# Optimization experiments

Hardware: AMD Instinct MI355X
Metric: run time of the kernel (lower is better)

Reference implementation:

```python
import jax, jax.numpy as jnp
import numpy as np

N_STEPS = 5
N_ETYPES = 4
N_GRAPHS = 64
HEADS = 2
N, E, D = 50000, 600000, 128
C = 32


def setup_inputs() -> dict:
    key = jax.random.key(0)
    ks = jax.random.split(key, 24)
    s = 0.08  # param scale to keep activations well-conditioned
    return {
        "in_feat1": jax.random.normal(ks[0], (N, D), jnp.float32),
        "in_feat2": jax.random.normal(ks[1], (N, D), jnp.float32),
        "src1": jax.random.randint(ks[2], (E,), 0, N, jnp.int32),
        "dst1": jax.random.randint(ks[3], (E,), 0, N, jnp.int32),
        "etype1": jax.random.randint(ks[4], (E,), 0, N_ETYPES, jnp.int32),
        "gid1": jnp.sort(jax.random.randint(ks[5], (N,), 0, N_GRAPHS, jnp.int32)),
        "src2": jax.random.randint(ks[6], (E,), 0, N, jnp.int32),
        "dst2": jax.random.randint(ks[7], (E,), 0, N, jnp.int32),
        "etype2": jax.random.randint(ks[8], (E,), 0, N_ETYPES, jnp.int32),
        "gid2": jnp.sort(jax.random.randint(ks[9], (N,), 0, N_GRAPHS, jnp.int32)),
        "W_et": jax.random.normal(ks[10], (N_ETYPES, D, D), jnp.float32) * s,
        "b_et": jax.random.normal(ks[11], (N_ETYPES, D), jnp.float32) * s,
        "W_ih": jax.random.normal(ks[12], (3 * D, D), jnp.float32) * s,
        "W_hh": jax.random.normal(ks[13], (3 * D, D), jnp.float32) * s,
        "b_ih": jax.random.normal(ks[14], (3 * D,), jnp.float32) * s,
        "b_hh": jax.random.normal(ks[15], (3 * D,), jnp.float32) * s,
        "W_fc": jax.random.normal(ks[16], (HEADS * D, D), jnp.float32) * s,
        "attn_l": jax.random.normal(ks[17], (HEADS, D), jnp.float32) * s,
        "attn_r": jax.random.normal(ks[18], (HEADS, D), jnp.float32) * s,
        "gat_bias": jax.random.normal(ks[19], (HEADS * D,), jnp.float32) * s,
        "W_cls": jax.random.normal(ks[20], (C, D), jnp.float32) * s,
        "b_cls": jax.random.normal(ks[21], (C,), jnp.float32) * s,
    }


def _ggann(feat, src, dst, etype, gid,
           W_et, b_et, W_ih, W_hh, b_ih, b_hh,
           W_fc, attn_l, attn_r, gat_bias, W_cls, b_cls):
    n = feat.shape[0]
    h = feat  # in_feats == out_feats -> no zero-padding needed
    # ---- GatedGraphConv: n_steps of per-etype message passing + GRU ----
    for _ in range(N_STEPS):
        # per-etype linear on all nodes: [K, N, D]
        t = jnp.einsum('kod,nd->kno', W_et, h) + b_et[:, None, :]
        msg = t[etype, src]                         # [E, D] gather by (etype, src)
        a = jax.ops.segment_sum(msg, dst, num_segments=n)  # [N, D]
        # GRUCell(a, h)
        gi = a @ W_ih.T + b_ih                      # [N, 3D]
        gh = h @ W_hh.T + b_hh
        i_r, i_z, i_n = jnp.split(gi, 3, axis=1)
        h_r, h_z, h_n = jnp.split(gh, 3, axis=1)
        r = jax.nn.sigmoid(i_r + h_r)
        z = jax.nn.sigmoid(i_z + h_z)
        nn_ = jnp.tanh(i_n + r * h_n)
        h = (1.0 - z) * nn_ + z * h
    # F.normalize (L2 over dim=1) then sigmoid
    h = h / jnp.maximum(jnp.linalg.norm(h, axis=1, keepdims=True), 1e-12)
    h = jax.nn.sigmoid(h)
    # ---- GATConv (num_heads=2) ----
    zft = (h @ W_fc.T).reshape(n, HEADS, D)         # [N, H, D]
    el = jnp.sum(zft * attn_l[None], axis=-1)       # [N, H]
    er = jnp.sum(zft * attn_r[None], axis=-1)
    e = jax.nn.leaky_relu(el[src] + er[dst], 0.2)   # [E, H]
    m = jax.ops.segment_max(e, dst, num_segments=n)
    ex = jnp.exp(e - m[dst])
    den = jax.ops.segment_sum(ex, dst, num_segments=n)
    alpha = ex / den[dst]                           # edge softmax per dst, per head
    rst = jax.ops.segment_sum(alpha[:, :, None] * zft[src], dst, num_segments=n)
    rst = rst + gat_bias.reshape(1, HEADS, D)
    h = jax.nn.relu(rst)                            # [N, H, D] (dropout = eval identity)
    # ---- mean_nodes per graph + classify ----
    sums = jax.ops.segment_sum(h, gid, num_segments=N_GRAPHS)      # [B, H, D]
    cnt = jax.ops.segment_sum(jnp.ones((n, 1, 1), h.dtype), gid, num_segments=N_GRAPHS)
    hg = sums / jnp.maximum(cnt, 1.0)
    return hg @ W_cls.T + b_cls                     # [B, H, C]


def reference(in_feat1, in_feat2, src1, dst1, etype1, gid1,
              src2, dst2, etype2, gid2,
              W_et, b_et, W_ih, W_hh, b_ih, b_hh,
              W_fc, attn_l, attn_r, gat_bias, W_cls, b_cls):
    params = (W_et, b_et, W_ih, W_hh, b_ih, b_hh,
              W_fc, attn_l, attn_r, gat_bias, W_cls, b_cls)
    h1 = _ggann(in_feat1, src1, dst1, etype1, gid1, *params)  # [B, H, C]
    h2 = _ggann(in_feat2, src2, dst2, etype2, gid2, *params)
    # F.pairwise_distance(p=2, eps=1e-6) over last dim -> [B, H]
    dist = jnp.linalg.norm(h1 - h2 + 1e-6, axis=-1)
    return jax.nn.softmax(dist, axis=1)             # softmax over the 2 heads
```

## Files before the change

kernel.cpp:

```cpp
#include <hip/hip_runtime.h>
#include <math.h>

#define D 128
#define NG 64
#define NG2 128
#define NSTEPS 5

using short8 = __attribute__((ext_vector_type(8))) short;
using f32x4  = __attribute__((ext_vector_type(4))) float;
using f32x2  = __attribute__((ext_vector_type(2))) float;

__device__ __forceinline__ float sigf(float x) {
  float e = __expf(-fabsf(x));
  float inv = __fdividef(1.f, 1.f + e);
  return x >= 0.f ? inv : e * inv;
}
__device__ __forceinline__ float tanhf_fast(float x) {
  float e = __expf(-2.f * fabsf(x));
  float r = (1.f - e) * __fdividef(1.f, 1.f + e);
  return x >= 0.f ? r : -r;
}
__device__ __forceinline__ float lrelu(float x) { return x > 0.f ? x : 0.2f * x; }
__device__ __forceinline__ short f2bf(float x) {
  unsigned u = __float_as_uint(x);
  u += 0x7fff + ((u >> 16) & 1);
  return (short)(u >> 16);
}
__device__ __forceinline__ unsigned pk2(float x, float y) {
  return ((unsigned)(unsigned short)f2bf(y) << 16) | (unsigned short)f2bf(x);
}
__device__ __forceinline__ float bflo(unsigned v) { return __uint_as_float(v << 16); }
__device__ __forceinline__ float bfhi(unsigned v) { return __uint_as_float(v & 0xffff0000u); }
__device__ __forceinline__ float bf2f(short s) {
  return __uint_as_float(((unsigned)(unsigned short)s) << 16);
}
__device__ __forceinline__ unsigned char f2fp8(float x) {
  int p = __builtin_amdgcn_cvt_pk_fp8_f32(x, x, 0, false);
  return (unsigned char)(p & 0xff);
}

__device__ __forceinline__ void packK128(const float* __restrict__ W,
                                         short* __restrict__ P, int i) {
  int j = i & 7;
  int lane = (i >> 3) & 63;
  int kt = (i >> 9) & 3;
  int nt = i >> 11;
  int c = nt * 16 + (lane & 15);
  int k = kt * 32 + ((lane >> 4) << 3) + j;
  P[i] = f2bf(W[c * 128 + k]);
}
__device__ __forceinline__ void packA512f(const float* __restrict__ W_et,
                                          short* __restrict__ P, int i) {
  int j = i & 7;
  int lane = (i >> 3) & 63;
  int kt = (i >> 9) & 15;
  int nt = i >> 13;
  int c = nt * 16 + (lane & 15);
  int k = kt * 32 + ((lane >> 4) << 3) + j;
  P[i] = f2bf(W_et[(k >> 7) * 16384 + c * 128 + (k & 127)]);
}

__global__ __launch_bounds__(256) void k_setup(const float* __restrict__ W_et,
    const float* __restrict__ W_ih, const float* __restrict__ W_hh,
    const float* __restrict__ W_fc, const float* __restrict__ f1,
    const float* __restrict__ f2, short* __restrict__ WaP, short* __restrict__ WihP,
    short* __restrict__ WhhP, short* __restrict__ WfcP, short* __restrict__ hb,
    unsigned char* __restrict__ hq,
    int* __restrict__ deg, int* __restrict__ gcnt, int N2, int Nd4) {
  const int sA = 65536, sB = 49152, sC = 49152, sD = 32768;
  int sE = N2, sF = NG2;
  long sG = 2L * Nd4;
  long tot = (long)(sA + sB + sC + sD) + sE + sF + sG;
  for (long ii = (long)blockIdx.x * blockDim.x + threadIdx.x; ii < tot;
       ii += (long)gridDim.x * blockDim.x) {
    long r = ii;
    if (r < sA) { packA512f(W_et, WaP, (int)r); continue; }
    r -= sA;
    if (r < sB) { packK128(W_ih, WihP, (int)r); continue; }
    r -= sB;
    if (r < sC) { packK128(W_hh, WhhP, (int)r); continue; }
    r -= sC;
    if (r < sD) { packK128(W_fc, WfcP, (int)r); continue; }
    r -= sD;
    if (r < sE) { deg[r] = 0; continue; }
    r -= sE;
    if (r < sF) { gcnt[r] = 0; continue; }
    r -= sF;
    {
      int i = (int)r;
      float4 v = (i < Nd4) ? ((const float4*)f1)[i] : ((const float4*)f2)[i - Nd4];
      ((uint2*)hb)[i] = make_uint2(pk2(v.x, v.y), pk2(v.z, v.w));
      int q = __builtin_amdgcn_cvt_pk_fp8_f32(v.x, v.y, 0, false);
      q = __builtin_amdgcn_cvt_pk_fp8_f32(v.z, v.w, q, true);
      ((unsigned*)hq)[i] = (unsigned)q;
    }
  }
}

__global__ __launch_bounds__(256) void k_histgid(const int* __restrict__ dst1,
    const int* __restrict__ dst2, const int* __restrict__ gid1,
    const int* __restrict__ gid2, int E, int N, int* __restrict__ deg,
    int* __restrict__ gidc, int* __restrict__ gcnt, int EB, int N2) {
  __shared__ int cnt[NG2];
  if ((int)blockIdx.x < EB) {
    int slice = blockIdx.x & 7;
    int bls = blockIdx.x >> 3;
    int nbs = EB >> 3;
    int W = (N2 + 7) >> 3;
    int lo = slice * W, hi = lo + W;
    for (int e = bls * 256 + threadIdx.x; e < 2 * E; e += nbs * 256) {
      int d = (e < E) ? dst1[e] : dst2[e - E] + N;
      if (d >= lo && d < hi) atomicAdd(&deg[d], 1);
    }
  } else {
    int t = threadIdx.x;
    if (t < NG2) cnt[t] = 0;
    __syncthreads();
    int i = (blockIdx.x - EB) * 256 + t;
    if (i < 2 * N) {
      int g = (i < N) ? gid1[i] : gid2[i - N] + NG;
      gidc[i] = g;
      atomicAdd(&cnt[g], 1);
    }
    __syncthreads();
    if (t < NG2 && cnt[t]) atomicAdd(&gcnt[t], cnt[t]);
  }
}

__global__ __launch_bounds__(256) void k_scan_a(const int* __restrict__ deg, int n,
                                                int* __restrict__ bsum) {
  int base = blockIdx.x * 1024 + threadIdx.x * 4;
  int s = 0;
  if (base + 3 < n) {
    int4 v = *(const int4*)(deg + base);
    s = v.x + v.y + v.z + v.w;
  } else {
    for (int k = 0; k < 4; ++k) if (base + k < n) s += deg[base + k];
  }
  #pragma unroll
  for (int off = 32; off; off >>= 1) s += __shfl_xor(s, off);
  __shared__ int ws[4];
  if ((threadIdx.x & 63) == 0) ws[threadIdx.x >> 6] = s;
  __syncthreads();
  if (threadIdx.x == 0) bsum[blockIdx.x] = ws[0] + ws[1] + ws[2] + ws[3];
}

__global__ __launch_bounds__(1024) void k_scan_b(const int* __restrict__ bsum,
                                                 int* __restrict__ boffs, int nb) {
  int tid = threadIdx.x;
  int v = (tid < nb) ? bsum[tid] : 0;
  int lane = tid & 63, wv = tid >> 6;
  int x = v;
  #pragma unroll
  for (int off = 1; off < 64; off <<= 1) {
    int y = __shfl_up(x, off);
    if (lane >= off) x += y;
  }
  __shared__ int wsum[16];
  if (lane == 63) wsum[wv] = x;
  __syncthreads();
  if (tid < 16) {
    int u = wsum[tid];
    #pragma unroll
    for (int off = 1; off < 16; off <<= 1) {
      int y = __shfl_up(u, off);
      if (tid >= off) u += y;
    }
    wsum[tid] = u;
  }
  __syncthreads();
  int woff = wv ? wsum[wv - 1] : 0;
  if (tid < nb) boffs[tid] = woff + x - v;
}

__global__ __launch_bounds__(256) void k_scan_c(const int* __restrict__ deg,
    const int* __restrict__ boffs, int* __restrict__ row_ofs,
    int* __restrict__ cursor, int n) {
  int base = blockIdx.x * 1024 + threadIdx.x * 4;
  int v[4] = {0, 0, 0, 0};
  if (base + 3 < n) {
    int4 t = *(const int4*)(deg + base);
    v[0] = t.x; v[1] = t.y; v[2] = t.z; v[3] = t.w;
  } else {
    for (int k = 0; k < 4; ++k) if (base + k < n) v[k] = deg[base + k];
  }
  int s = v[0] + v[1] + v[2] + v[3];
  int lane = threadIdx.x & 63, wv = threadIdx.x >> 6;
  int x = s;
  #pragma unroll
  for (int off = 1; off < 64; off <<= 1) {
    int y = __shfl_up(x, off);
    if (lane >= off) x += y;
  }
  __shared__ int wsum[4];
  if (lane == 63) wsum[wv] = x;
  __syncthreads();
  int woff = 0;
  for (int w = 0; w < wv; ++w) woff += wsum[w];
  int run = boffs[blockIdx.x] + woff + x - s;
  #pragma unroll
  for (int k = 0; k < 4; ++k) {
    int i = base + k;
    if (i < n) {
      cursor[i] = run;
      run += v[k];
      row_ofs[i + 1] = run;
    }
  }
  if (blockIdx.x == 0 && threadIdx.x == 0) row_ofs[0] = 0;
}

__global__ __launch_bounds__(256) void k_scatter(const int* __restrict__ src1,
    const int* __restrict__ dst1, const int* __restrict__ ety1,
    const int* __restrict__ src2, const int* __restrict__ dst2,
    const int* __restrict__ ety2, int E, int N, int* __restrict__ cursor,
    int* __restrict__ csr_se, int N2) {
  int slice = blockIdx.x & 7;
  int bls = blockIdx.x >> 3;
  int nbs = gridDim.x >> 3;
  int W = (N2 + 7) >> 3;
  int lo = slice * W, hi = lo + W;
  for (int e = bls * 256 + threadIdx.x; e < 2 * E; e += nbs * 256) {
    int d = (e < E) ? dst1[e] : dst2[e - E] + N;
    if (d < lo || d >= hi) continue;
    int s, et;
    if (e < E) { s = src1[e]; et = ety1[e]; }
    else { s = src2[e - E] + N; et = ety2[e - E]; }
    int p = atomicAdd(&cursor[d], 1);
    csr_se[p] = (s << 10) + et;
  }
}

__global__ __launch_bounds__(1024) void k_aggemm(const unsigned char* __restrict__ hq,
    const int* __restrict__ row_ofs, const int* __restrict__ csr_se,
    const short* __restrict__ WaP, const float* __restrict__ b_et,
    short* __restrict__ ab, int M) {
  __shared__ short Stile[16 * 512];
  __shared__ float lcnt[16][4];
  int tid = threadIdx.x;
  int lane = tid & 63, wave = tid >> 6;
  int row0 = blockIdx.x * 16;

  int li = wave;
  int node = row0 + li;
  f32x2 A0 = {0.f, 0.f}, A1 = {0.f, 0.f}, A2 = {0.f, 0.f}, A3 = {0.f, 0.f};
  int c0 = 0, c1 = 0, c2 = 0, c3 = 0;
  const char* hqb = (const char*)hq;
  if (node < M) {
    int beg = row_ofs[node], end = row_ofs[node + 1];
    #define ACC(ET, V) do { \
        f32x2 t_ = __builtin_amdgcn_cvt_pk_f32_fp8((unsigned)(V), false); \
        if (ET == 0)      { A0 += t_; ++c0; } \
        else if (ET == 1) { A1 += t_; ++c1; } \
        else if (ET == 2) { A2 += t_; ++c2; } \
        else              { A3 += t_; ++c3; } } while (0)
    for (int base = beg; base < end; base += 64) {
      int nv = end - base; if (nv > 64) nv = 64;
      int r = (lane < nv) ? csr_se[base + lane] : 0;
      int j = 0;
      for (; j + 16 <= nv; j += 16) {
        int rr[16];
        #pragma unroll
        for (int k = 0; k < 16; ++k) rr[k] = __builtin_amdgcn_readlane(r, j + k);
        unsigned short v[16];
        #pragma unroll
        for (int k = 0; k < 16; ++k)
          v[k] = ((const unsigned short*)(hqb + (rr[k] >> 3)))[lane];
        #pragma unroll
        for (int k = 0; k < 16; ++k) ACC(rr[k] & 3, v[k]);
      }
      for (; j + 8 <= nv; j += 8) {
        int rr[8];
        #pragma unroll
        for (int k = 0; k < 8; ++k) rr[k] = __builtin_amdgcn_readlane(r, j + k);
        unsigned short v[8];
        #pragma unroll
        for (int k = 0; k < 8; ++k)
          v[k] = ((const unsigned short*)(hqb + (rr[k] >> 3)))[lane];
        #pragma unroll
        for (int k = 0; k < 8; ++k) ACC(rr[k] & 3, v[k]);
      }
      for (; j + 4 <= nv; j += 4) {
        int rr[4];
        #pragma unroll
        for (int k = 0; k < 4; ++k) rr[k] = __builtin_amdgcn_readlane(r, j + k);
        unsigned short v[4];
        #pragma unroll
        for (int k = 0; k < 4; ++k)
          v[k] = ((const unsigned short*)(hqb + (rr[k] >> 3)))[lane];
        #pragma unroll
        for (int k = 0; k < 4; ++k) ACC(rr[k] & 3, v[k]);
      }
      for (; j < nv; ++j) {
        int rr = __builtin_amdgcn_readlane(r, j);
        unsigned short v = ((const unsigned short*)(hqb + (rr >> 3)))[lane];
        ACC(rr & 3, v);
      }
    }
    #undef ACC
  }
  {
    int swz = (li & 7) << 4;
    unsigned* ld = (unsigned*)Stile;
    ld[(li * 1024 + ((lane * 4      ) ^ swz)) >> 2] = pk2(A0[0], A0[1]);
    ld[(li * 1024 + ((lane * 4 + 256) ^ swz)) >> 2] = pk2(A1[0], A1[1]);
    ld[(li * 1024 + ((lane * 4 + 512) ^ swz)) >> 2] = pk2(A2[0], A2[1]);
    ld[(li * 1024 + ((lane * 4 + 768) ^ swz)) >> 2] = pk2(A3[0], A3[1]);
    if (lane == 0) {
      lcnt[li][0] = (float)c0; lcnt[li][1] = (float)c1;
      lcnt[li][2] = (float)c2; lcnt[li][3] = (float)c3;
    }
  }
  __syncthreads();

  if (wave < 8) {
    int quad = lane >> 4, l15 = lane & 15;
    int swz = (l15 & 7) << 4;
    int nt = wave;
    f32x4 acc = {0.f, 0.f, 0.f, 0.f};
    #pragma unroll
    for (int kt = 0; kt < 16; ++kt) {
      int boff = l15 * 1024 + ((kt * 64 + quad * 16) ^ swz);
      short8 a = *(const short8*)((const char*)Stile + boff);
      short8 b = *(const short8*)(WaP + (((size_t)(nt * 16 + kt) * 64) + lane) * 8);
      acc = __builtin_amdgcn_mfma_f32_16x16x32_bf16(a, b, acc, 0, 0, 0);
    }
    int c = nt * 16 + l15;
    float be0 = b_et[c], be1 = b_et[128 + c], be2 = b_et[256 + c], be3 = b_et[384 + c];
    #pragma unroll
    for (int reg = 0; reg < 4; ++reg) {
      int lr = quad * 4 + reg;
      int r = row0 + lr;
      if (r < M) {
        float v = acc[reg] + lcnt[lr][0] * be0 + lcnt[lr][1] * be1
                           + lcnt[lr][2] * be2 + lcnt[lr][3] * be3;
        ab[(size_t)r * 128 + c] = f2bf(v);
      }
    }
  }
}

__global__ __launch_bounds__(256) void k_gru_mfma(const short* __restrict__ ab,
    short* __restrict__ hb, unsigned char* __restrict__ hq,
    const short* __restrict__ Pih, const short* __restrict__ Phh,
    const float* __restrict__ b_ih, const float* __restrict__ b_hh, int M) {
  int tid = threadIdx.x;
  int lane = tid & 63, wave = tid >> 6;
  int row0 = blockIdx.x * 128 + wave * 32;
  int quad = lane >> 4, l15 = lane & 15;
  short8 fa[2][4], fh[2][4];
  #pragma unroll
  for (int rt = 0; rt < 2; ++rt) {
    int ar = row0 + rt * 16 + l15; if (ar >= M) ar = M - 1;
    #pragma unroll
    for (int kt = 0; kt < 4; ++kt) {
      fa[rt][kt] = *(const short8*)(ab + (size_t)ar * 128 + kt * 32 + quad * 8);
      fh[rt][kt] = *(const short8*)(hb + (size_t)ar * 128 + kt * 32 + quad * 8);
    }
  }
  for (int nt = 0; nt < 8; ++nt) {
    f32x4 accr[2], accz[2], acci[2], acch[2];
    #pragma unroll
    for (int rt = 0; rt < 2; ++rt) {
      accr[rt] = {0.f,0.f,0.f,0.f}; accz[rt] = {0.f,0.f,0.f,0.f};
      acci[rt] = {0.f,0.f,0.f,0.f}; acch[rt] = {0.f,0.f,0.f,0.f};
    }
    #pragma unroll
    for (int kt = 0; kt < 4; ++kt) {
      size_t li = ((size_t)lane) * 8;
      short8 wr = *(const short8*)(Pih + ((size_t)((nt     ) * 4 + kt) * 64) * 8 + li);
      short8 wz = *(const short8*)(Pih + ((size_t)((nt +  8) * 4 + kt) * 64) * 8 + li);
      short8 wn = *(const short8*)(Pih + ((size_t)((nt + 16) * 4 + kt) * 64) * 8 + li);
      short8 ur = *(const short8*)(Phh + ((size_t)((nt     ) * 4 + kt) * 64) * 8 + li);
      short8 uz = *(const short8*)(Phh + ((size_t)((nt +  8) * 4 + kt) * 64) * 8 + li);
      short8 un = *(const short8*)(Phh + ((size_t)((nt + 16) * 4 + kt) * 64) * 8 + li);
      #pragma unroll
      for (int rt = 0; rt < 2; ++rt) {
        accr[rt] = __builtin_amdgcn_mfma_f32_16x16x32_bf16(fa[rt][kt], wr, accr[rt], 0, 0, 0);
        accr[rt] = __builtin_amdgcn_mfma_f32_16x16x32_bf16(fh[rt][kt], ur, accr[rt], 0, 0, 0);
        accz[rt] = __builtin_amdgcn_mfma_f32_16x16x32_bf16(fa[rt][kt], wz, accz[rt], 0, 0, 0);
        accz[rt] = __builtin_amdgcn_mfma_f32_16x16x32_bf16(fh[rt][kt], uz, accz[rt], 0, 0, 0);
        acci[rt] = __builtin_amdgcn_mfma_f32_16x16x32_bf16(fa[rt][kt], wn, acci[rt], 0, 0, 0);
        acch[rt] = __builtin_amdgcn_mfma_f32_16x16x32_bf16(fh[rt][kt], un, acch[rt], 0, 0, 0);
      }
    }
    int c = nt * 16 + l15;
    float bir = b_ih[c],      bhr = b_hh[c];
    float biz = b_ih[c+128],  bhz = b_hh[c+128];
    float bin_= b_ih[c+256],  bhn = b_hh[c+256];
    #pragma unroll
    for (int rt = 0; rt < 2; ++rt) {
      #pragma unroll
      for (int reg = 0; reg < 4; ++reg) {
        int r = row0 + rt * 16 + quad * 4 + reg;
        if (r < M) {
          float rg = sigf(accr[rt][reg] + bir + bhr);
          float zg = sigf(accz[rt][reg] + biz + bhz);
          float ng = tanhf_fast(acci[rt][reg] + bin_ + rg * (acch[rt][reg] + bhn));
          float hold = bf2f(hb[(size_t)r * 128 + c]);
          float hn2 = (1.f - zg) * ng + zg * hold;
          hb[(size_t)r * 128 + c] = f2bf(hn2);
          hq[(size_t)r * 128 + c] = f2fp8(hn2);
        }
      }
    }
  }
}

__global__ __launch_bounds__(256) void k_fc_eler(const short* __restrict__ Ab,
    const short* __restrict__ Bp, const float* __restrict__ attn_l,
    const float* __restrict__ attn_r, unsigned char* __restrict__ zq,
    float* __restrict__ el, float* __restrict__ er, int M) {
  int tid = threadIdx.x;
  int lane = tid & 63, wave = tid >> 6;
  int row0 = blockIdx.x * 128 + wave * 32;
  int quad = lane >> 4, l15 = lane & 15;
  short8 af[2][4];
  #pragma unroll
  for (int rt = 0; rt < 2; ++rt) {
    int ar = row0 + rt * 16 + l15; if (ar >= M) ar = M - 1;
    #pragma unroll
    for (int kt = 0; kt < 4; ++kt)
      af[rt][kt] = *(const short8*)(Ab + (size_t)ar * 128 + kt * 32 + quad * 8);
  }
  #pragma unroll
  for (int rt = 0; rt < 2; ++rt) {
    float ss = 0.f;
    #pragma unroll
    for (int kt = 0; kt < 4; ++kt)
      #pragma unroll
      for (int j = 0; j < 8; ++j) {
        float x = bf2f(af[rt][kt][j]);
        ss += x * x;
      }
    ss += __shfl_xor(ss, 16);
    ss += __shfl_xor(ss, 32);
    float inv = 1.f / fmaxf(sqrtf(ss), 1e-12f);
    #pragma unroll
    for (int kt = 0; kt < 4; ++kt)
      #pragma unroll
      for (int j = 0; j < 8; ++j)
        af[rt][kt][j] = f2bf(sigf(bf2f(af[rt][kt][j]) * inv));
  }
  float elp[2][2][4] = {};
  float erp[2][2][4] = {};
  for (int nt = 0; nt < 16; ++nt) {
    f32x4 a0 = {0.f,0.f,0.f,0.f}, a1 = {0.f,0.f,0.f,0.f};
    #pragma unroll
    for (int kt = 0; kt < 4; ++kt) {
      short8 b = *(const short8*)(Bp + (((size_t)(nt * 4 + kt) * 64) + lane) * 8);
      a0 = __builtin_amdgcn_mfma_f32_16x16x32_bf16(af[0][kt], b, a0, 0, 0, 0);
      a1 = __builtin_amdgcn_mfma_f32_16x16x32_bf16(af[1][kt], b, a1, 0, 0, 0);
    }
    int head = nt >> 3;
    int colh = (nt & 7) * 16 + l15;
    float alv = attn_l[head * 128 + colh];
    float arv = attn_r[head * 128 + colh];
    int c = nt * 16 + l15;
    #pragma unroll
    for (int rt = 0; rt < 2; ++rt) {
      f32x4 acc = rt ? a1 : a0;
      #pragma unroll
      for (int reg = 0; reg < 4; ++reg) {
        int r = row0 + rt * 16 + quad * 4 + reg;
        if (r < M) zq[(size_t)r * 256 + c] = f2fp8(acc[reg]);
        elp[rt][head][reg] += acc[reg] * alv;
        erp[rt][head][reg] += acc[reg] * arv;
      }
    }
  }
  #pragma unroll
  for (int off = 1; off < 16; off <<= 1) {
    #pragma unroll
    for (int rt = 0; rt < 2; ++rt)
      #pragma unroll
      for (int h = 0; h < 2; ++h)
        #pragma unroll
        for (int reg = 0; reg < 4; ++reg) {
          elp[rt][h][reg] += __shfl_xor(elp[rt][h][reg], off);
          erp[rt][h][reg] += __shfl_xor(erp[rt][h][reg], off);
        }
  }
  if (l15 == 0) {
    #pragma unroll
    for (int rt = 0; rt < 2; ++rt)
      #pragma unroll
      for (int h = 0; h < 2; ++h)
        #pragma unroll
        for (int reg = 0; reg < 4; ++reg) {
          int r = row0 + rt * 16 + quad * 4 + reg;
          if (r < M) {
            el[r * 2 + h] = elp[rt][h][reg];
            er[r * 2 + h] = erp[rt][h][reg];
          }
        }
  }
}

__global__ __launch_bounds__(256) void k_gat(const unsigned char* __restrict__ zq,
    const float* __restrict__ el, const float* __restrict__ er,
    const int* __restrict__ row_ofs, const int* __restrict__ csr_se,
    const float* __restrict__ gat_bias, short* __restrict__ outb,
    float* __restrict__ sums, int N) {
  if (blockIdx.x < NG2) sums[blockIdx.x * 256 + threadIdx.x] = 0.f;
  int node = blockIdx.x * 4 + (threadIdx.x >> 6);
  int lane = threadIdx.x & 63;
  if (node >= N) return;
  int beg = row_ofs[node], end = row_ofs[node + 1];
  float2 ern = ((const float2*)er)[node];
  float l0 = 0.f, l1 = 0.f;
  float4 acc = {0.f, 0.f, 0.f, 0.f};
  int head = lane >> 5;
  const char* elb = (const char*)el;
  const char* zqb = (const char*)zq;
  for (int base = beg; base < end; base += 64) {
    int nv = end - base; if (nv > 64) nv = 64;
    int se = (lane < nv) ? csr_se[base + lane] : 0;
    float p0 = 0.f, p1 = 0.f;
    if (lane < nv) {
      float2 els = *(const float2*)(elb + (se >> 7));
      p0 = expf(lrelu(els.x + ern.x));
      p1 = expf(lrelu(els.y + ern.y));
    }
    float t0 = p0, t1 = p1;
    #pragma unroll
    for (int off = 32; off; off >>= 1) { t0 += __shfl_xor(t0, off); t1 += __shfl_xor(t1, off); }
    l0 += t0; l1 += t1;
    int w01 = (int)pk2(p0, p1);
    int j = 0;
    for (; j + 8 <= nv; j += 8) {
      int bb[8]; unsigned ww[8];
      #pragma unroll
      for (int k = 0; k < 8; ++k) {
        bb[k] = __builtin_amdgcn_readlane(se, j + k) >> 2;
        ww[k] = (unsigned)__builtin_amdgcn_readlane(w01, j + k);
      }
      unsigned zz[8];
      #pragma unroll
      for (int k = 0; k < 8; ++k)
        zz[k] = ((const unsigned*)(zqb + bb[k]))[lane];
      #pragma unroll
      for (int k = 0; k < 8; ++k) {
        float f = head ? bfhi(ww[k]) : bflo(ww[k]);
        f32x2 lo = __builtin_amdgcn_cvt_pk_f32_fp8(zz[k], false);
        f32x2 hi = __builtin_amdgcn_cvt_pk_f32_fp8(zz[k], true);
        acc.x += f * lo[0]; acc.y += f * lo[1];
        acc.z += f * hi[0]; acc.w += f * hi[1];
      }
    }
    for (; j + 4 <= nv; j += 4) {
      int bb[4]; unsigned ww[4];
      #pragma unroll
      for (int k = 0; k < 4; ++k) {
        bb[k] = __builtin_amdgcn_readlane(se, j + k) >> 2;
        ww[k] = (unsigned)__builtin_amdgcn_readlane(w01, j + k);
      }
      unsigned zz[4];
      #pragma unroll
      for (int k = 0; k < 4; ++k)
        zz[k] = ((const unsigned*)(zqb + bb[k]))[lane];
      #pragma unroll
      for (int k = 0; k < 4; ++k) {
        float f = head ? bfhi(ww[k]) : bflo(ww[k]);
        f32x2 lo = __builtin_amdgcn_cvt_pk_f32_fp8(zz[k], false);
        f32x2 hi = __builtin_amdgcn_cvt_pk_f32_fp8(zz[k], true);
        acc.x += f * lo[0]; acc.y += f * lo[1];
        acc.z += f * hi[0]; acc.w += f * hi[1];
      }
    }
    for (; j < nv; ++j) {
      int bj = __builtin_amdgcn_readlane(se, j) >> 2;
      unsigned wj = (unsigned)__builtin_amdgcn_readlane(w01, j);
      float w = head ? bfhi(wj) : bflo(wj);
      unsigned zv = ((const unsigned*)(zqb + bj))[lane];
      f32x2 lo = __builtin_amdgcn_cvt_pk_f32_fp8(zv, false);
      f32x2 hi = __builtin_amdgcn_cvt_pk_f32_fp8(zv, true);
      acc.x += w * lo[0]; acc.y += w * lo[1];
      acc.z += w * hi[0]; acc.w += w * hi[1];
    }
  }
  float inv0 = (l0 > 0.f) ? 1.f / l0 : 0.f;
  float inv1 = (l1 > 0.f) ? 1.f / l1 : 0.f;
  float inv = head ? inv1 : inv0;
  float4 b = ((const float4*)gat_bias)[lane];
  float ox = fmaxf(acc.x * inv + b.x, 0.f);
  float oy = fmaxf(acc.y * inv + b.y, 0.f);
  float oz = fmaxf(acc.z * inv + b.z, 0.f);
  float ow = fmaxf(acc.w * inv + b.w, 0.f);
  ((uint2*)(outb + (size_t)node * 256))[lane] = make_uint2(pk2(ox, oy), pk2(oz, ow));
}

__global__ __launch_bounds__(256) void k_segred(const short* __restrict__ hgatb,
    const int* __restrict__ gidc, float* __restrict__ sums, int NT2) {
  int node0 = blockIdx.x * 128;
  int col = threadIdx.x;
  int end = node0 + 128; if (end > NT2) end = NT2;
  if (node0 >= NT2) return;
  float acc = 0.f;
  int gcur = gidc[node0];
  for (int n = node0; n < end; ++n) {
    int g = gidc[n];
    if (g != gcur) {
      atomicAdd(&sums[gcur * 256 + col], acc);
      acc = 0.f; gcur = g;
    }
    acc += bf2f(hgatb[(size_t)n * 256 + col]);
  }
  atomicAdd(&sums[gcur * 256 + col], acc);
}

__global__ __launch_bounds__(64) void k_classify(const float* __restrict__ sums,
    const int* __restrict__ gcnt, const float* __restrict__ W_cls,
    const float* __restrict__ b_cls, float* __restrict__ logits) {
  int g = blockIdx.x, tid = threadIdx.x;
  int hh = tid >> 5, c = tid & 31;
  float invc = 1.f / fmaxf((float)gcnt[g], 1.f);
  float acc = 0.f;
  for (int d = 0; d < D; ++d)
    acc += (sums[g * 256 + hh * D + d] * invc) * W_cls[c * D + d];
  logits[g * 64 + hh * 32 + c] = acc + b_cls[c];
}

__global__ __launch_bounds__(64) void k_final(const float* __restrict__ logits,
    float* __restrict__ out) {
  int g = threadIdx.x;
  if (g >= NG) return;
  float d[2];
  #pragma unroll
  for (int hh = 0; hh < 2; ++hh) {
    float s = 0.f;
    for (int c = 0; c < 32; ++c) {
      float df = logits[g * 64 + hh * 32 + c] - logits[(g + NG) * 64 + hh * 32 + c] + 1e-6f;
      s += df * df;
    }
    d[hh] = sqrtf(s);
  }
  float mx = fmaxf(d[0], d[1]);
  float e0 = expf(d[0] - mx), e1 = expf(d[1] - mx);
  float den = e0 + e1;
  out[g * 2] = e0 / den;
  out[g * 2 + 1] = e1 / den;
}

extern "C" void kernel_launch(void* const* d_in, const int* in_sizes, int n_in,
                              void* d_out, int out_size, void* d_ws, size_t ws_size,
                              hipStream_t stream) {
  const float* in_feat1 = (const float*)d_in[0];
  const float* in_feat2 = (const float*)d_in[1];
  const int* src1 = (const int*)d_in[2];
  const int* dst1 = (const int*)d_in[3];
  const int* ety1 = (const int*)d_in[4];
  const int* gid1 = (const int*)d_in[5];
  const int* src2 = (const int*)d_in[6];
  const int* dst2 = (const int*)d_in[7];
  const int* ety2 = (const int*)d_in[8];
  const int* gid2 = (const int*)d_in[9];
  const float* W_et = (const float*)d_in[10];
  const float* b_et = (const float*)d_in[11];
  const float* W_ih = (const float*)d_in[12];
  const float* W_hh = (const float*)d_in[13];
  const float* b_ih = (const float*)d_in[14];
  const float* b_hh = (const float*)d_in[15];
  const float* W_fc = (const float*)d_in[16];
  const float* attn_l = (const float*)d_in[17];
  const float* attn_r = (const float*)d_in[18];
  const float* gat_bias = (const float*)d_in[19];
  const float* W_cls = (const float*)d_in[20];
  const float* b_cls = (const float*)d_in[21];
  float* out = (float*)d_out;

  int N = in_sizes[0] / D;
  int E = in_sizes[2];
  int N2 = 2 * N, E2 = 2 * E;

  char* p = (char*)d_ws;
  auto alloc = [&](size_t bytes) -> void* {
    char* r = p;
    p += (bytes + 255) & ~(size_t)255;
    return (void*)r;
  };
  short* WaP  = (short*)alloc((size_t)512 * 128 * 2);
  short* WihP = (short*)alloc((size_t)384 * 128 * 2);
  short* WhhP = (short*)alloc((size_t)384 * 128 * 2);
  short* WfcP = (short*)alloc((size_t)256 * 128 * 2);
  short* hb  = (short*)alloc((size_t)N2 * D * 2);
  unsigned char* hq = (unsigned char*)alloc((size_t)N2 * D);
  short* ab  = (short*)alloc((size_t)N2 * D * 2);
  short* hgatb = (short*)alloc((size_t)N2 * 256 * 2);
  unsigned char* zq = (unsigned char*)alloc((size_t)N2 * 256);
  float* el  = (float*)alloc((size_t)N2 * 2 * 4);
  float* er  = (float*)alloc((size_t)N2 * 2 * 4);
  float* sums= (float*)alloc((size_t)NG2 * 256 * 4);
  float* logits = (float*)alloc((size_t)NG2 * 64 * 4);
  int* deg     = (int*)alloc((size_t)N2 * 4);
  int* row_ofs = (int*)alloc(((size_t)N2 + 1) * 4);
  int* cursor  = (int*)alloc((size_t)N2 * 4);
  int* gidc    = (int*)alloc((size_t)N2 * 4);
  int* gcnt    = (int*)alloc((size_t)NG2 * 4);
  int* bsum    = (int*)alloc((size_t)1024 * 4);
  int* boffs   = (int*)alloc((size_t)1024 * 4);
  int* csr_se  = (int*)alloc((size_t)E2 * 4);
  if ((size_t)(p - (char*)d_ws) > ws_size) return;

  k_setup<<<dim3(2048), dim3(256), 0, stream>>>(W_et, W_ih, W_hh, W_fc,
      in_feat1, in_feat2, WaP, WihP, WhhP, WfcP, hb, hq, deg, gcnt, N2, N * D / 4);

  int EB = 4800;
  int GB = (N2 + 255) / 256;
  int nb = (N2 + 1023) / 1024;
  k_histgid<<<dim3(EB + GB), dim3(256), 0, stream>>>(dst1, dst2, gid1, gid2,
                                                     E, N, deg, gidc, gcnt, EB, N2);
  k_scan_a<<<dim3(nb), dim3(256), 0, stream>>>(deg, N2, bsum);
  k_scan_b<<<dim3(1), dim3(1024), 0, stream>>>(bsum, boffs, nb);
  k_scan_c<<<dim3(nb), dim3(256), 0, stream>>>(deg, boffs, row_ofs, cursor, N2);
  k_scatter<<<dim3(4800), dim3(256), 0, stream>>>(src1, dst1, ety1, src2, dst2, ety2,
                                                  E, N, cursor, csr_se, N2);

  int gb16 = (N2 + 15) / 16;
  int gb128 = (N2 + 127) / 128;
  int nb4 = (N2 + 3) / 4;

  for (int s = 0; s < NSTEPS; ++s) {
    k_aggemm<<<dim3(gb16), dim3(1024), 0, stream>>>(hq, row_ofs, csr_se, WaP, b_et, ab, N2);
    k_gru_mfma<<<dim3(gb128), dim3(256), 0, stream>>>(ab, hb, hq, WihP, WhhP, b_ih, b_hh, N2);
  }
  k_fc_eler<<<dim3(gb128), dim3(256), 0, stream>>>(hb, WfcP, attn_l, attn_r, zq, el, er, N2);
  k_gat<<<dim3(nb4), dim3(256), 0, stream>>>(zq, el, er, row_ofs, csr_se,
                                             gat_bias, hgatb, sums, N2);
  k_segred<<<dim3((N2 + 127) / 128), dim3(256), 0, stream>>>(hgatb, gidc, sums, N2);
  k_classify<<<dim3(NG2), dim3(64), 0, stream>>>(sums, gcnt, W_cls, b_cls, logits);
  k_final<<<dim3(1), dim3(64), 0, stream>>>(logits, out);
}
```

Measured before the change: 1.197 ms.

## Stage GRU outputs in LDS for coalesced stores and halve rows per wave

The GRU kernel now handles 16 rows per wave instead of 32, so it launches twice as many blocks. It writes the new hidden state (bf16 and fp8) into shared memory first and then stores it to global memory as coalesced 16-byte vectors, replacing the scattered 2-byte and 1-byte stores. The aim is to improve store efficiency and occupancy. In exchange, each weight fragment loaded from global memory is reused across half as many rows, so weight-load traffic per row doubles.

```diff
diff --git a/kernel.cpp b/kernel.cpp
--- a/kernel.cpp
+++ b/kernel.cpp
@@ -344,27 +344,22 @@
     short* __restrict__ hb, unsigned char* __restrict__ hq,
     const short* __restrict__ Pih, const short* __restrict__ Phh,
     const float* __restrict__ b_ih, const float* __restrict__ b_hh, int M) {
+  __shared__ short hbs[4][16 * 128];
+  __shared__ unsigned char hqs[4][16 * 128];
   int tid = threadIdx.x;
   int lane = tid & 63, wave = tid >> 6;
-  int row0 = blockIdx.x * 128 + wave * 32;
+  int row0 = blockIdx.x * 64 + wave * 16;
   int quad = lane >> 4, l15 = lane & 15;
-  short8 fa[2][4], fh[2][4];
-  #pragma unroll
-  for (int rt = 0; rt < 2; ++rt) {
-    int ar = row0 + rt * 16 + l15; if (ar >= M) ar = M - 1;
-    #pragma unroll
-    for (int kt = 0; kt < 4; ++kt) {
-      fa[rt][kt] = *(const short8*)(ab + (size_t)ar * 128 + kt * 32 + quad * 8);
-      fh[rt][kt] = *(const short8*)(hb + (size_t)ar * 128 + kt * 32 + quad * 8);
-    }
+  short8 fa[4], fh[4];
+  int ar = row0 + l15; if (ar >= M) ar = M - 1;
+  #pragma unroll
+  for (int kt = 0; kt < 4; ++kt) {
+    fa[kt] = *(const short8*)(ab + (size_t)ar * 128 + kt * 32 + quad * 8);
+    fh[kt] = *(const short8*)(hb + (size_t)ar * 128 + kt * 32 + quad * 8);
   }
   for (int nt = 0; nt < 8; ++nt) {
-    f32x4 accr[2], accz[2], acci[2], acch[2];
-    #pragma unroll
-    for (int rt = 0; rt < 2; ++rt) {
-      accr[rt] = {0.f,0.f,0.f,0.f}; accz[rt] = {0.f,0.f,0.f,0.f};
-      acci[rt] = {0.f,0.f,0.f,0.f}; acch[rt] = {0.f,0.f,0.f,0.f};
-    }
+    f32x4 accr = {0.f,0.f,0.f,0.f}, accz = {0.f,0.f,0.f,0.f};
+    f32x4 acci = {0.f,0.f,0.f,0.f}, acch = {0.f,0.f,0.f,0.f};
     #pragma unroll
     for (int kt = 0; kt < 4; ++kt) {
       size_t li = ((size_t)lane) * 8;
@@ -374,35 +369,47 @@
       short8 ur = *(const short8*)(Phh + ((size_t)((nt     ) * 4 + kt) * 64) * 8 + li);
       short8 uz = *(const short8*)(Phh + ((size_t)((nt +  8) * 4 + kt) * 64) * 8 + li);
       short8 un = *(const short8*)(Phh + ((size_t)((nt + 16) * 4 + kt) * 64) * 8 + li);
-      #pragma unroll
-      for (int rt = 0; rt < 2; ++rt) {
-        accr[rt] = __builtin_amdgcn_mfma_f32_16x16x32_bf16(fa[rt][kt], wr, accr[rt], 0, 0, 0);
-        accr[rt] = __builtin_amdgcn_mfma_f32_16x16x32_bf16(fh[rt][kt], ur, accr[rt], 0, 0, 0);
-        accz[rt] = __builtin_amdgcn_mfma_f32_16x16x32_bf16(fa[rt][kt], wz, accz[rt], 0, 0, 0);
-        accz[rt] = __builtin_amdgcn_mfma_f32_16x16x32_bf16(fh[rt][kt], uz, accz[rt], 0, 0, 0);
-        acci[rt] = __builtin_amdgcn_mfma_f32_16x16x32_bf16(fa[rt][kt], wn, acci[rt], 0, 0, 0);
-        acch[rt] = __builtin_amdgcn_mfma_f32_16x16x32_bf16(fh[rt][kt], un, acch[rt], 0, 0, 0);
-      }
+      accr = __builtin_amdgcn_mfma_f32_16x16x32_bf16(fa[kt], wr, accr, 0, 0, 0);
+      accr = __builtin_amdgcn_mfma_f32_16x16x32_bf16(fh[kt], ur, accr, 0, 0, 0);
+      accz = __builtin_amdgcn_mfma_f32_16x16x32_bf16(fa[kt], wz, accz, 0, 0, 0);
+      accz = __builtin_amdgcn_mfma_f32_16x16x32_bf16(fh[kt], uz, accz, 0, 0, 0);
+      acci = __builtin_amdgcn_mfma_f32_16x16x32_bf16(fa[kt], wn, acci, 0, 0, 0);
+      acch = __builtin_amdgcn_mfma_f32_16x16x32_bf16(fh[kt], un, acch, 0, 0, 0);
     }
     int c = nt * 16 + l15;
     float bir = b_ih[c],      bhr = b_hh[c];
     float biz = b_ih[c+128],  bhz = b_hh[c+128];
     float bin_= b_ih[c+256],  bhn = b_hh[c+256];
     #pragma unroll
-    for (int rt = 0; rt < 2; ++rt) {
-      #pragma unroll
-      for (int reg = 0; reg < 4; ++reg) {
-        int r = row0 + rt * 16 + quad * 4 + reg;
-        if (r < M) {
-          float rg = sigf(accr[rt][reg] + bir + bhr);
-          float zg = sigf(accz[rt][reg] + biz + bhz);
-          float ng = tanhf_fast(acci[rt][reg] + bin_ + rg * (acch[rt][reg] + bhn));
-          float hold = bf2f(hb[(size_t)r * 128 + c]);
-          float hn2 = (1.f - zg) * ng + zg * hold;
-          hb[(size_t)r * 128 + c] = f2bf(hn2);
-          hq[(size_t)r * 128 + c] = f2fp8(hn2);
-        }
-      }
+    for (int reg = 0; reg < 4; ++reg) {
+      int lr = quad * 4 + reg;
+      int r = row0 + lr;
+      float rg = sigf(accr[reg] + bir + bhr);
+      float zg = sigf(accz[reg] + biz + bhz);
+      float ng = tanhf_fast(acci[reg] + bin_ + rg * (acch[reg] + bhn));
+      float hold = (r < M) ? bf2f(hb[(size_t)r * 128 + c]) : 0.f;
+      float hn2 = (1.f - zg) * ng + zg * hold;
+      hbs[wave][lr * 128 + c] = f2bf(hn2);
+      hqs[wave][lr * 128 + c] = f2fp8(hn2);
+    }
+  }
+  size_t gbase = (size_t)row0 * 128;
+  #pragma unroll
+  for (int i = 0; i < 4; ++i) {
+    int gshort = i * 512 + lane * 8;
+    int grow = gshort >> 7;
+    if (row0 + grow < M) {
+      uint4 v = *(const uint4*)&hbs[wave][gshort];
+      *(uint4*)(hb + gbase + gshort) = v;
+    }
+  }
+  #pragma unroll
+  for (int i = 0; i < 2; ++i) {
+    int gbyte = i * 1024 + lane * 16;
+    int grow = gbyte >> 7;
+    if (row0 + grow < M) {
+      uint4 v = *(const uint4*)&hqs[wave][gbyte];
+      *(uint4*)(hq + gbase + gbyte) = v;
     }
   }
 }
@@ -717,12 +724,13 @@
                                                   E, N, cursor, csr_se, N2);
 
   int gb16 = (N2 + 15) / 16;
+  int gb64 = (N2 + 63) / 64;
   int gb128 = (N2 + 127) / 128;
   int nb4 = (N2 + 3) / 4;
 
   for (int s = 0; s < NSTEPS; ++s) {
     k_aggemm<<<dim3(gb16), dim3(1024), 0, stream>>>(hq, row_ofs, csr_se, WaP, b_et, ab, N2);
-    k_gru_mfma<<<dim3(gb128), dim3(256), 0, stream>>>(ab, hb, hq, WihP, WhhP, b_ih, b_hh, N2);
+    k_gru_mfma<<<dim3(gb64), dim3(256), 0, stream>>>(ab, hb, hq, WihP, WhhP, b_ih, b_hh, N2);
   }
   k_fc_eler<<<dim3(gb128), dim3(256), 0, stream>>>(hb, WfcP, attn_l, attn_r, zq, el, er, N2);
   k_gat<<<dim3(nb4), dim3(256), 0, stream>>>(zq, el, er, row_ofs, csr_se,
```

Measured after the change: 1.184 ms. About the same (-1.1%).
